# Optimization experiments

Hardware: AMD Instinct MI355X
Metric: run time of the kernel (lower is better)

Reference implementation:

```python
import jax, jax.numpy as jnp
import numpy as np

B, C, D, H, W = 4, 128, 16, 16, 16
C8 = C // 8
TEXT = 256
N = D * H * W


def setup_inputs() -> dict:
    key = jax.random.key(0)
    ks = jax.random.split(key, 13)
    s = lambda fan: 1.0 / np.sqrt(fan)
    return {
        "x": jax.random.normal(ks[0], (B, C, D, H, W), jnp.float32),
        "text_emb": jax.random.normal(ks[1], (B, TEXT), jnp.float32),
        "Wq": jax.random.normal(ks[2], (C8, C), jnp.float32) * s(C),
        "bq": jax.random.normal(ks[3], (C8,), jnp.float32) * 0.01,
        "Wk": jax.random.normal(ks[4], (C8, C), jnp.float32) * s(C),
        "bk": jax.random.normal(ks[5], (C8,), jnp.float32) * 0.01,
        "Wv": jax.random.normal(ks[6], (C, C), jnp.float32) * s(C),
        "bv": jax.random.normal(ks[7], (C,), jnp.float32) * 0.01,
        "Wtk": jax.random.normal(ks[8], (C8, TEXT), jnp.float32) * s(TEXT),
        "btk": jax.random.normal(ks[9], (C8,), jnp.float32) * 0.01,
        "Wtv": jax.random.normal(ks[10], (C, TEXT), jnp.float32) * s(TEXT),
        "btv": jax.random.normal(ks[11], (C,), jnp.float32) * 0.01,
        # gamma is zero-init in the original; use a nonzero value so the
        # attention path contributes to the output (and to gradients).
        "gamma": jax.random.normal(ks[12], (1,), jnp.float32) * 0.1 + 0.5,
    }


def reference(x, text_emb, Wq, bq, Wk, bk, Wv, bv, Wtk, btk, Wtv, btv, gamma):
    b, c, d, h, w = x.shape
    n = d * h * w
    xf = x.reshape(b, c, n)                       # [B, C, N]
    # 1x1x1 convs == channel matmuls
    q = jnp.einsum('oc,bcn->bno', Wq, xf) + bq    # [B, N, C8]
    k = jnp.einsum('oc,bcn->bon', Wk, xf) + bk[None, :, None]  # [B, C8, N]
    v = jnp.einsum('oc,bcn->bon', Wv, xf) + bv[None, :, None]  # [B, C, N]
    # text-conditioned additive key/value (broadcast over all voxels)
    tk = (text_emb @ Wtk.T + btk)[:, :, None]     # [B, C8, 1]
    tv = (text_emb @ Wtv.T + btv)[:, :, None]     # [B, C, 1]
    k = k + tk
    v = v + tv
    # unscaled attention: softmax over keys
    scores = jnp.einsum('bno,bom->bnm', q, k)     # [B, N, N]
    attn = jax.nn.softmax(scores, axis=-1)
    # out[b,c,n] = sum_m v[b,c,m] * attn[b,n,m]
    out = jnp.einsum('bcm,bnm->bcn', v, attn).reshape(b, c, d, h, w)
    return gamma * out + x
```

## Files before the change

### kernel.cpp

```cpp
#include <hip/hip_runtime.h>
#include <math.h>

#define BB 4
#define CC 128
#define C8 16
#define TEXTN 256
#define NN 4096
#define WQB 64
#define NT 32

typedef __attribute__((ext_vector_type(8))) __bf16 bf16x8;
typedef __attribute__((ext_vector_type(16))) float f32x16;

#define LOG2E 1.44269504088896340736f

static __device__ __forceinline__ ushort f2bf(float f) {
  unsigned u = __builtin_bit_cast(unsigned, f);
  u += 0x7FFFu + ((u >> 16) & 1u);
  return (ushort)(u >> 16);
}

static __device__ __forceinline__ float exp2a(float x) {
#if __has_builtin(__builtin_amdgcn_exp2f)
  return __builtin_amdgcn_exp2f(x);
#else
  return exp2f(x);
#endif
}

static __device__ __forceinline__ unsigned cvt_pk_bf16(float lo, float hi) {
  unsigned r;
  asm("v_cvt_pk_bf16_f32 %0, %1, %2" : "=v"(r) : "v"(lo), "v"(hi));
  return r;
}
static __device__ __forceinline__ void pl32swap(unsigned &a, unsigned &b) {
  asm("v_permlane32_swap_b32 %0, %1" : "+v"(a), "+v"(b));
}

__global__ __launch_bounds__(256) void k_text(
    const float* __restrict__ text, const float* __restrict__ Wtk,
    const float* __restrict__ btk, const float* __restrict__ Wtv,
    const float* __restrict__ btv, float* __restrict__ tkv) {
  __shared__ float ts[TEXTN];
  int b = blockIdx.x;
  for (int i = threadIdx.x; i < TEXTN; i += 256) ts[i] = text[b * TEXTN + i];
  __syncthreads();
  int o = threadIdx.x;
  if (o < 144) {
    const float* w;
    float acc;
    if (o < 16) { w = Wtk + o * TEXTN; acc = btk[o]; }
    else        { w = Wtv + (o - 16) * TEXTN; acc = btv[o - 16]; }
    #pragma unroll 8
    for (int t = 0; t < TEXTN; t++) acc += w[t] * ts[t];
    tkv[b * 144 + o] = acc;
  }
}

__global__ __launch_bounds__(320) void k_qkv(
    const float* __restrict__ x,
    const float* __restrict__ Wq, const float* __restrict__ bq,
    const float* __restrict__ Wk, const float* __restrict__ bk,
    const float* __restrict__ Wv, const float* __restrict__ bv,
    const float* __restrict__ tkv,
    ushort* __restrict__ qt, ushort* __restrict__ kt, ushort* __restrict__ vtB) {
  __shared__ __align__(16) ushort xs[64 * 128];
  int b = blockIdx.x >> 6;
  int n0 = (blockIdx.x & 63) * 64;
  int t = threadIdx.x;
  int w = t >> 6, lane = t & 63, l31 = lane & 31, hi = lane >> 5;

  for (int i = t; i < 1024; i += 320) {
    int n = i & 63, ch = i >> 6;
    union { ushort u[8]; uint4 v; } pk;
    #pragma unroll
    for (int j = 0; j < 8; ++j)
      pk.u[j] = f2bf(x[((size_t)b * CC + ch * 8 + j) * NN + n0 + n]);
    *(uint4*)&xs[n * 128 + ((ch ^ (n & 15)) << 3)] = pk.v;
  }

  const float* wrow;
  if (w == 0) wrow = (l31 < 16) ? (Wq + l31 * CC) : (Wk + (l31 - 16) * CC);
  else        wrow = Wv + (size_t)(32 * (w - 1) + l31) * CC;
  bf16x8 af[8];
  #pragma unroll
  for (int ks = 0; ks < 8; ++ks) {
    float4 u0 = *(const float4*)&wrow[ks * 16 + hi * 8];
    float4 u1 = *(const float4*)&wrow[ks * 16 + hi * 8 + 4];
    union { ushort u[8]; bf16x8 v; } tmp;
    tmp.u[0] = f2bf(u0.x); tmp.u[1] = f2bf(u0.y); tmp.u[2] = f2bf(u0.z); tmp.u[3] = f2bf(u0.w);
    tmp.u[4] = f2bf(u1.x); tmp.u[5] = f2bf(u1.y); tmp.u[6] = f2bf(u1.z); tmp.u[7] = f2bf(u1.w);
    af[ks] = tmp.v;
  }
  float badd[16];
  #pragma unroll
  for (int r = 0; r < 16; ++r) {
    int ol = (r & 3) + 8 * (r >> 2) + 4 * hi;
    if (w == 0) badd[r] = (ol < 16) ? bq[ol] : (bk[ol - 16] + tkv[b * 144 + ol - 16]);
    else { int c = 32 * (w - 1) + ol; badd[r] = bv[c] + tkv[b * 144 + 16 + c]; }
  }
  __syncthreads();

  #pragma unroll
  for (int n32 = 0; n32 < 2; ++n32) {
    int n = n32 * 32 + l31;
    int ng = n0 + n;
    bf16x8 bf[8];
    #pragma unroll
    for (int ks = 0; ks < 8; ++ks)
      bf[ks] = *(const bf16x8*)&xs[n * 128 + (((ks * 2 + hi) ^ (n & 15)) << 3)];
    f32x16 d;
    #pragma unroll
    for (int r = 0; r < 16; ++r) d[r] = 0.f;
    #pragma unroll
    for (int ks = 0; ks < 8; ++ks)
      d = __builtin_amdgcn_mfma_f32_32x32x16_bf16(af[ks], bf[ks], d, 0, 0, 0);
    #pragma unroll
    for (int g = 0; g < 4; ++g) {
      int o0 = 8 * g + 4 * hi;
      float v0 = d[g * 4 + 0] + badd[g * 4 + 0];
      float v1 = d[g * 4 + 1] + badd[g * 4 + 1];
      float v2 = d[g * 4 + 2] + badd[g * 4 + 2];
      float v3 = d[g * 4 + 3] + badd[g * 4 + 3];
      if (w == 0 && o0 < 16) { v0 *= LOG2E; v1 *= LOG2E; v2 *= LOG2E; v3 *= LOG2E; }
      ushort4 pkv;
      pkv.x = f2bf(v0); pkv.y = f2bf(v1); pkv.z = f2bf(v2); pkv.w = f2bf(v3);
      if (w == 0) {
        if (o0 < 16) *(ushort4*)&qt[(b * NN + ng) * C8 + o0] = pkv;
        else         *(ushort4*)&kt[(b * NN + ng) * C8 + o0 - 16] = pkv;
      } else {
        int c0 = 32 * (w - 1) + o0;
        int base = b * (NN / 8) * CC * 8 + (ng >> 3) * (CC * 8) + (ng & 7);
        vtB[base + (c0 + 0) * 8] = pkv.x;
        vtB[base + (c0 + 1) * 8] = pkv.y;
        vtB[base + (c0 + 2) * 8] = pkv.z;
        vtB[base + (c0 + 3) * 8] = pkv.w;
      }
    }
  }
}

__global__ __launch_bounds__(512) void k_attn(
    const ushort* __restrict__ qt, const ushort* __restrict__ kt,
    const ushort* __restrict__ vtB, const float* __restrict__ x,
    const float* __restrict__ gamma_p, float* __restrict__ out) {
  __shared__ __align__(16) float mergeAcc[4][2][1024];
  __shared__ float mergeL[4][2][2][32];
  __shared__ float invGL[64];

  int b = blockIdx.x >> 6;
  int q0 = (blockIdx.x & 63) * WQB;
  int t = threadIdx.x;
  int w = t >> 6, lane = t & 63, l31 = lane & 31, hi = lane >> 5;
  int ms = w >> 1, ch = w & 1;

  const ushort* ktb = kt + (size_t)b * NN * C8;
  const ushort* vbb = vtB + (size_t)b * (NN / 8) * CC * 8;

  bf16x8 qfA = *(const bf16x8*)&qt[((size_t)b * NN + q0 + l31) * C8 + hi * 8];
  bf16x8 qfB = *(const bf16x8*)&qt[((size_t)b * NN + q0 + 32 + l31) * C8 + hi * 8];

  f32x16 accA0, accA1, accB0, accB1;
  #pragma unroll
  for (int r = 0; r < 16; ++r) { accA0[r] = 0.f; accA1[r] = 0.f; accB0[r] = 0.f; accB1[r] = 0.f; }
  float lpA = 0.f, lpB = 0.f;

  f32x16 z;
  #pragma unroll
  for (int r = 0; r < 16; ++r) z[r] = 0.f;

  const ushort* kp  = ktb + (ms * 32 + l31) * C8 + hi * 8;
  const ushort* vp0 = vbb + (size_t)(ms * 4 + 0 + hi) * (CC * 8) + (ch * 64 + l31) * 8;
  const ushort* vp1 = vbb + (size_t)(ms * 4 + 2 + hi) * (CC * 8) + (ch * 64 + l31) * 8;

  bf16x8 kfA, kfB;
  kfA = *(const bf16x8*)kp; kp += 128 * C8;

#define MKPF(P, OUT0, OUT1)                                                   \
  {                                                                           \
    unsigned a0 = cvt_pk_bf16(P[0], P[1]), b0 = cvt_pk_bf16(P[4], P[5]);      \
    unsigned c0 = cvt_pk_bf16(P[2], P[3]), d0 = cvt_pk_bf16(P[6], P[7]);      \
    pl32swap(a0, b0); pl32swap(c0, d0);                                       \
    union { unsigned u[4]; bf16x8 v; } u0; u0.u[0] = a0; u0.u[1] = c0;        \
    u0.u[2] = b0; u0.u[3] = d0; OUT0 = u0.v;                                  \
    unsigned a1 = cvt_pk_bf16(P[8], P[9]), b1 = cvt_pk_bf16(P[12], P[13]);    \
    unsigned c1 = cvt_pk_bf16(P[10], P[11]), d1 = cvt_pk_bf16(P[14], P[15]);  \
    pl32swap(a1, b1); pl32swap(c1, d1);                                       \
    union { unsigned u[4]; bf16x8 v; } u1; u1.u[0] = a1; u1.u[1] = c1;        \
    u1.u[2] = b1; u1.u[3] = d1; OUT1 = u1.v;                                  \
  }

#define STEP(CK, NK)                                                          \
  {                                                                           \
    NK = *(const bf16x8*)kp; kp += 128 * C8;                                  \
    bf16x8 vA0 = *(const bf16x8*)(vp0);                   \
    bf16x8 vA1 = *(const bf16x8*)(vp0 + 256);             \
    bf16x8 vB0 = *(const bf16x8*)(vp1);                   \
    bf16x8 vB1 = *(const bf16x8*)(vp1 + 256);             \
    vp0 += 16 * CC * 8; vp1 += 16 * CC * 8;                                   \
    f32x16 sA = __builtin_amdgcn_mfma_f32_32x32x16_bf16(CK, qfA, z, 0, 0, 0); \
    f32x16 sB = __builtin_amdgcn_mfma_f32_32x32x16_bf16(CK, qfB, z, 0, 0, 0); \
    float pA[16], pB[16];                                                     \
    _Pragma("unroll")                                                         \
    for (int r = 0; r < 16; ++r) pA[r] = exp2a(sA[r]);                        \
    _Pragma("unroll")                                                         \
    for (int r = 0; r < 16; ++r) pB[r] = exp2a(sB[r]);                        \
    {                                                                         \
      float y0 = (pA[0] + pA[1]) + (pA[2] + pA[3]);                           \
      float y1 = (pA[4] + pA[5]) + (pA[6] + pA[7]);                           \
      float y2 = (pA[8] + pA[9]) + (pA[10] + pA[11]);                         \
      float y3 = (pA[12] + pA[13]) + (pA[14] + pA[15]);                       \
      lpA += (y0 + y1) + (y2 + y3);                                           \
      float u0 = (pB[0] + pB[1]) + (pB[2] + pB[3]);                           \
      float u1 = (pB[4] + pB[5]) + (pB[6] + pB[7]);                           \
      float u2 = (pB[8] + pB[9]) + (pB[10] + pB[11]);                         \
      float u3 = (pB[12] + pB[13]) + (pB[14] + pB[15]);                       \
      lpB += (u0 + u1) + (u2 + u3);                                           \
    }                                                                         \
    bf16x8 pfA0, pfA1, pfB0, pfB1;                                            \
    MKPF(pA, pfA0, pfA1)                                                      \
    MKPF(pB, pfB0, pfB1)                                                      \
    __builtin_amdgcn_s_setprio(1);                                            \
    accA0 = __builtin_amdgcn_mfma_f32_32x32x16_bf16(vA0, pfA0, accA0, 0, 0, 0); \
    accA1 = __builtin_amdgcn_mfma_f32_32x32x16_bf16(vA1, pfA0, accA1, 0, 0, 0); \
    accB0 = __builtin_amdgcn_mfma_f32_32x32x16_bf16(vA0, pfB0, accB0, 0, 0, 0); \
    accB1 = __builtin_amdgcn_mfma_f32_32x32x16_bf16(vA1, pfB0, accB1, 0, 0, 0); \
    accA0 = __builtin_amdgcn_mfma_f32_32x32x16_bf16(vB0, pfA1, accA0, 0, 0, 0); \
    accA1 = __builtin_amdgcn_mfma_f32_32x32x16_bf16(vB1, pfA1, accA1, 0, 0, 0); \
    accB0 = __builtin_amdgcn_mfma_f32_32x32x16_bf16(vB0, pfB1, accB0, 0, 0, 0); \
    accB1 = __builtin_amdgcn_mfma_f32_32x32x16_bf16(vB1, pfB1, accB1, 0, 0, 0); \
    __builtin_amdgcn_s_setprio(0);                                            \
  }

  for (int tt = 0; tt < NT; tt += 2) {
    STEP(kfA, kfB)
    STEP(kfB, kfA)
  }
#undef STEP
#undef MKPF

  if (ch == 0) {
    mergeL[ms][hi][0][l31] = lpA;
    mergeL[ms][hi][1][l31] = lpB;
  }
  __syncthreads();
  if (t < 64) {
    float L = 0.f;
    #pragma unroll
    for (int m2 = 0; m2 < 4; ++m2)
      #pragma unroll
      for (int h2 = 0; h2 < 2; ++h2) L += mergeL[m2][h2][t >> 5][t & 31];
    invGL[t] = gamma_p[0] / L;
  }

#define EPI(ACC, QT, CB, FIRST)                                               \
  {                                                                           \
    if (!(FIRST)) __syncthreads();                                            \
    _Pragma("unroll")                                                         \
    for (int r = 0; r < 16; ++r)                                              \
      mergeAcc[ms][ch][(((r & 3) + 8 * (r >> 2) + 4 * hi) << 5) | l31] = ACC[r]; \
    __syncthreads();                                                          \
    int idx = t * 4;                                                          \
    int qq = idx & 31, cl = idx >> 5;                                         \
    int chh = cl >> 5, crow = cl & 31;                                        \
    float4 sum = *(const float4*)&mergeAcc[0][chh][crow * 32 + qq];           \
    _Pragma("unroll")                                                         \
    for (int m2 = 1; m2 < 4; ++m2) {                                          \
      float4 sv = *(const float4*)&mergeAcc[m2][chh][crow * 32 + qq];         \
      sum.x += sv.x; sum.y += sv.y; sum.z += sv.z; sum.w += sv.w;             \
    }                                                                         \
    float4 gl = *(const float4*)&invGL[(QT) * 32 + qq];                       \
    int c = chh * 64 + (CB) * 32 + crow;                                      \
    size_t base = ((size_t)b * CC + c) * NN + q0 + (QT) * 32 + qq;            \
    float4 xv = *(const float4*)&x[base];                                     \
    float4 ov;                                                                \
    ov.x = sum.x * gl.x + xv.x;                                               \
    ov.y = sum.y * gl.y + xv.y;                                               \
    ov.z = sum.z * gl.z + xv.z;                                               \
    ov.w = sum.w * gl.w + xv.w;                                               \
    *(float4*)&out[base] = ov;                                                \
  }

  EPI(accA0, 0, 0, 1)
  EPI(accA1, 0, 1, 0)
  EPI(accB0, 1, 0, 0)
  EPI(accB1, 1, 1, 0)
#undef EPI
}

extern "C" void kernel_launch(void* const* d_in, const int* in_sizes, int n_in,
                              void* d_out, int out_size, void* d_ws, size_t ws_size,
                              hipStream_t stream) {
  const float* x     = (const float*)d_in[0];
  const float* text  = (const float*)d_in[1];
  const float* Wq    = (const float*)d_in[2];
  const float* bq    = (const float*)d_in[3];
  const float* Wk    = (const float*)d_in[4];
  const float* bk    = (const float*)d_in[5];
  const float* Wv    = (const float*)d_in[6];
  const float* bv    = (const float*)d_in[7];
  const float* Wtk   = (const float*)d_in[8];
  const float* btk   = (const float*)d_in[9];
  const float* Wtv   = (const float*)d_in[10];
  const float* btv   = (const float*)d_in[11];
  const float* gamma = (const float*)d_in[12];
  float* outp = (float*)d_out;

  char* wsb = (char*)d_ws;
  float*  tkv = (float*)wsb;
  ushort* qt  = (ushort*)(wsb + 4096);
  ushort* kt  = (ushort*)(wsb + 4096 + 524288);
  ushort* vtB = (ushort*)(wsb + 4096 + 2 * 524288);

  k_text<<<BB, 256, 0, stream>>>(text, Wtk, btk, Wtv, btv, tkv);
  k_qkv<<<BB * NN / 64, 320, 0, stream>>>(x, Wq, bq, Wk, bk, Wv, bv, tkv, qt, kt, vtB);
  k_attn<<<BB * NN / WQB, 512, 0, stream>>>(qt, kt, vtB, x, gamma, outp);
}
```

Measured before the change: 52.89 us.

## Split attention over channel halves with LDS-staged V and shared P tiles

Doubles the attention grid by splitting output channels into two halves per block. Each warp now computes scores for one 32-query tile instead of two and shares its bf16 probabilities through LDS. V tiles are double-buffered into LDS with global_load_lds instead of being read directly from global memory. Block indices are swizzled across XCDs. The aim is more parallelism and less per-warp exp/score work, at the cost of a barrier every key step and recomputing QK scores and exps once for each channel half.

```diff
diff --git a/kernel.cpp b/kernel.cpp
--- a/kernel.cpp
+++ b/kernel.cpp
@@ -35,6 +35,12 @@
 }
 static __device__ __forceinline__ void pl32swap(unsigned &a, unsigned &b) {
   asm("v_permlane32_swap_b32 %0, %1" : "+v"(a), "+v"(b));
+}
+
+static __device__ __forceinline__ void gl_lds16(const ushort* g, ushort* l) {
+  __builtin_amdgcn_global_load_lds(
+      (const __attribute__((address_space(1))) unsigned*)g,
+      (__attribute__((address_space(3))) unsigned*)l, 16, 0, 0);
 }
 
 __global__ __launch_bounds__(256) void k_text(
@@ -144,133 +150,135 @@
     const ushort* __restrict__ qt, const ushort* __restrict__ kt,
     const ushort* __restrict__ vtB, const float* __restrict__ x,
     const float* __restrict__ gamma_p, float* __restrict__ out) {
-  __shared__ __align__(16) float mergeAcc[4][2][1024];
-  __shared__ float mergeL[4][2][2][32];
-  __shared__ float invGL[64];
-
-  int b = blockIdx.x >> 6;
-  int q0 = (blockIdx.x & 63) * WQB;
+  __shared__ __align__(16) char smem[49152];
+  ushort* Vb = (ushort*)smem;
+  ushort* Pb = (ushort*)(smem + 32768);
+  float* mergeAcc = (float*)smem;
+  float* mergeLf  = (float*)(smem + 32768);
+  float* invGLf   = (float*)(smem + 32768 + 2048);
+
+  int raw = blockIdx.x;
+  int swz = (raw & 7) * 64 + (raw >> 3);
+  int b = swz >> 7, chalf = (swz >> 6) & 1, q0 = (swz & 63) * WQB;
   int t = threadIdx.x;
   int w = t >> 6, lane = t & 63, l31 = lane & 31, hi = lane >> 5;
   int ms = w >> 1, ch = w & 1;
 
-  const ushort* ktb = kt + (size_t)b * NN * C8;
-  const ushort* vbb = vtB + (size_t)b * (NN / 8) * CC * 8;
-
-  bf16x8 qfA = *(const bf16x8*)&qt[((size_t)b * NN + q0 + l31) * C8 + hi * 8];
-  bf16x8 qfB = *(const bf16x8*)&qt[((size_t)b * NN + q0 + 32 + l31) * C8 + hi * 8];
-
-  f32x16 accA0, accA1, accB0, accB1;
-  #pragma unroll
-  for (int r = 0; r < 16; ++r) { accA0[r] = 0.f; accA1[r] = 0.f; accB0[r] = 0.f; accB1[r] = 0.f; }
-  float lpA = 0.f, lpB = 0.f;
+  const ushort* ktb  = kt + (size_t)b * NN * C8;
+  const ushort* vsrc = vtB + (size_t)b * (NN / 8) * CC * 8 + chalf * 64 * 8;
+
+  bf16x8 qf = *(const bf16x8*)&qt[((size_t)b * NN + q0 + ch * 32 + l31) * C8 + hi * 8];
+
+  f32x16 acc0, acc1;
+  #pragma unroll
+  for (int r = 0; r < 16; ++r) { acc0[r] = 0.f; acc1[r] = 0.f; }
+  float lp = 0.f;
 
   f32x16 z;
   #pragma unroll
   for (int r = 0; r < 16; ++r) z[r] = 0.f;
 
-  const ushort* kp  = ktb + (ms * 32 + l31) * C8 + hi * 8;
-  const ushort* vp0 = vbb + (size_t)(ms * 4 + 0 + hi) * (CC * 8) + (ch * 64 + l31) * 8;
-  const ushort* vp1 = vbb + (size_t)(ms * 4 + 2 + hi) * (CC * 8) + (ch * 64 + l31) * 8;
-
-  bf16x8 kfA, kfB;
-  kfA = *(const bf16x8*)kp; kp += 128 * C8;
-
-#define MKPF(P, OUT0, OUT1)                                                   \
+#define STAGE(STEP, BUF)                                                      \
   {                                                                           \
-    unsigned a0 = cvt_pk_bf16(P[0], P[1]), b0 = cvt_pk_bf16(P[4], P[5]);      \
-    unsigned c0 = cvt_pk_bf16(P[2], P[3]), d0 = cvt_pk_bf16(P[6], P[7]);      \
-    pl32swap(a0, b0); pl32swap(c0, d0);                                       \
-    union { unsigned u[4]; bf16x8 v; } u0; u0.u[0] = a0; u0.u[1] = c0;        \
-    u0.u[2] = b0; u0.u[3] = d0; OUT0 = u0.v;                                  \
-    unsigned a1 = cvt_pk_bf16(P[8], P[9]), b1 = cvt_pk_bf16(P[12], P[13]);    \
-    unsigned c1 = cvt_pk_bf16(P[10], P[11]), d1 = cvt_pk_bf16(P[14], P[15]);  \
-    pl32swap(a1, b1); pl32swap(c1, d1);                                       \
-    union { unsigned u[4]; bf16x8 v; } u1; u1.u[0] = a1; u1.u[1] = c1;        \
-    u1.u[2] = b1; u1.u[3] = d1; OUT1 = u1.v;                                  \
-  }
-
-#define STEP(CK, NK)                                                          \
-  {                                                                           \
-    NK = *(const bf16x8*)kp; kp += 128 * C8;                                  \
-    bf16x8 vA0 = *(const bf16x8*)(vp0);                   \
-    bf16x8 vA1 = *(const bf16x8*)(vp0 + 256);             \
-    bf16x8 vB0 = *(const bf16x8*)(vp1);                   \
-    bf16x8 vB1 = *(const bf16x8*)(vp1 + 256);             \
-    vp0 += 16 * CC * 8; vp1 += 16 * CC * 8;                                   \
-    f32x16 sA = __builtin_amdgcn_mfma_f32_32x32x16_bf16(CK, qfA, z, 0, 0, 0); \
-    f32x16 sB = __builtin_amdgcn_mfma_f32_32x32x16_bf16(CK, qfB, z, 0, 0, 0); \
-    float pA[16], pB[16];                                                     \
-    _Pragma("unroll")                                                         \
-    for (int r = 0; r < 16; ++r) pA[r] = exp2a(sA[r]);                        \
-    _Pragma("unroll")                                                         \
-    for (int r = 0; r < 16; ++r) pB[r] = exp2a(sB[r]);                        \
-    {                                                                         \
-      float y0 = (pA[0] + pA[1]) + (pA[2] + pA[3]);                           \
-      float y1 = (pA[4] + pA[5]) + (pA[6] + pA[7]);                           \
-      float y2 = (pA[8] + pA[9]) + (pA[10] + pA[11]);                         \
-      float y3 = (pA[12] + pA[13]) + (pA[14] + pA[15]);                       \
-      lpA += (y0 + y1) + (y2 + y3);                                           \
-      float u0 = (pB[0] + pB[1]) + (pB[2] + pB[3]);                           \
-      float u1 = (pB[4] + pB[5]) + (pB[6] + pB[7]);                           \
-      float u2 = (pB[8] + pB[9]) + (pB[10] + pB[11]);                         \
-      float u3 = (pB[12] + pB[13]) + (pB[14] + pB[15]);                       \
-      lpB += (u0 + u1) + (u2 + u3);                                           \
-    }                                                                         \
-    bf16x8 pfA0, pfA1, pfB0, pfB1;                                            \
-    MKPF(pA, pfA0, pfA1)                                                      \
-    MKPF(pB, pfB0, pfB1)                                                      \
-    __builtin_amdgcn_s_setprio(1);                                            \
-    accA0 = __builtin_amdgcn_mfma_f32_32x32x16_bf16(vA0, pfA0, accA0, 0, 0, 0); \
-    accA1 = __builtin_amdgcn_mfma_f32_32x32x16_bf16(vA1, pfA0, accA1, 0, 0, 0); \
-    accB0 = __builtin_amdgcn_mfma_f32_32x32x16_bf16(vA0, pfB0, accB0, 0, 0, 0); \
-    accB1 = __builtin_amdgcn_mfma_f32_32x32x16_bf16(vA1, pfB0, accB1, 0, 0, 0); \
-    accA0 = __builtin_amdgcn_mfma_f32_32x32x16_bf16(vB0, pfA1, accA0, 0, 0, 0); \
-    accA1 = __builtin_amdgcn_mfma_f32_32x32x16_bf16(vB1, pfA1, accA1, 0, 0, 0); \
-    accB0 = __builtin_amdgcn_mfma_f32_32x32x16_bf16(vB0, pfB1, accB0, 0, 0, 0); \
-    accB1 = __builtin_amdgcn_mfma_f32_32x32x16_bf16(vB1, pfB1, accB1, 0, 0, 0); \
-    __builtin_amdgcn_s_setprio(0);                                            \
-  }
-
-  for (int tt = 0; tt < NT; tt += 2) {
-    STEP(kfA, kfB)
-    STEP(kfB, kfA)
-  }
-#undef STEP
-#undef MKPF
-
-  if (ch == 0) {
-    mergeL[ms][hi][0][l31] = lpA;
-    mergeL[ms][hi][1][l31] = lpB;
-  }
+    int cg = (STEP) << 4;                                                     \
+    gl_lds16(vsrc + ((size_t)(cg + (t >> 6)) * CC + (t & 63)) * 8,            \
+             Vb + (BUF) * 8192 + t * 8);                                      \
+    gl_lds16(vsrc + ((size_t)(cg + 8 + (t >> 6)) * CC + (t & 63)) * 8,        \
+             Vb + (BUF) * 8192 + (t + 512) * 8);                              \
+  }
+
+#define LDK(T) (*(const bf16x8*)&ktb[((T) * 128 + ms * 32 + l31) * C8 + hi * 8])
+#define LDVF(CUR, KS) (*(const bf16x8*)&Vb[(CUR) * 8192 + ((ms * 4 + (KS) * 2 + hi) * 64 + (ch * 32 + l31)) * 8])
+#define PSLOT(MS, QT, KS) ((bf16x8*)&Pb[((((MS) * 2 + (QT)) * 2 + (KS)) * 64 + lane) * 8])
+
+  STAGE(0, 0)
+  bf16x8 kf = LDK(0);
+  __syncthreads();
+
+  for (int tt = 0; tt < NT; ++tt) {
+    int cur = tt & 1;
+    int tn = (tt + 1) & (NT - 1);
+    STAGE(tn, cur ^ 1)
+    bf16x8 kfn = LDK(tn);
+    bf16x8 vf0 = LDVF(cur, 0);
+    bf16x8 vf1 = LDVF(cur, 1);
+
+    f32x16 s = __builtin_amdgcn_mfma_f32_32x32x16_bf16(kf, qf, z, 0, 0, 0);
+    float p[16];
+    #pragma unroll
+    for (int r = 0; r < 16; ++r) p[r] = exp2a(s[r]);
+    {
+      float y0 = (p[0] + p[1]) + (p[2] + p[3]);
+      float y1 = (p[4] + p[5]) + (p[6] + p[7]);
+      float y2 = (p[8] + p[9]) + (p[10] + p[11]);
+      float y3 = (p[12] + p[13]) + (p[14] + p[15]);
+      lp += (y0 + y1) + (y2 + y3);
+    }
+    {
+      unsigned a0 = cvt_pk_bf16(p[0], p[1]), b0 = cvt_pk_bf16(p[4], p[5]);
+      unsigned c0 = cvt_pk_bf16(p[2], p[3]), d0 = cvt_pk_bf16(p[6], p[7]);
+      pl32swap(a0, b0); pl32swap(c0, d0);
+      union { unsigned u[4]; bf16x8 v; } u0; u0.u[0] = a0; u0.u[1] = c0;
+      u0.u[2] = b0; u0.u[3] = d0;
+      *PSLOT(ms, ch, 0) = u0.v;
+      unsigned a1 = cvt_pk_bf16(p[8], p[9]), b1 = cvt_pk_bf16(p[12], p[13]);
+      unsigned c1 = cvt_pk_bf16(p[10], p[11]), d1 = cvt_pk_bf16(p[14], p[15]);
+      pl32swap(a1, b1); pl32swap(c1, d1);
+      union { unsigned u[4]; bf16x8 v; } u1; u1.u[0] = a1; u1.u[1] = c1;
+      u1.u[2] = b1; u1.u[3] = d1;
+      *PSLOT(ms, ch, 1) = u1.v;
+    }
+    asm volatile("s_waitcnt lgkmcnt(0)" ::: "memory");
+    __builtin_amdgcn_s_barrier();
+
+    bf16x8 pA0 = *PSLOT(ms, 0, 0);
+    bf16x8 pA1 = *PSLOT(ms, 0, 1);
+    bf16x8 pB0 = *PSLOT(ms, 1, 0);
+    bf16x8 pB1 = *PSLOT(ms, 1, 1);
+
+    __builtin_amdgcn_s_setprio(1);
+    acc0 = __builtin_amdgcn_mfma_f32_32x32x16_bf16(vf0, pA0, acc0, 0, 0, 0);
+    acc0 = __builtin_amdgcn_mfma_f32_32x32x16_bf16(vf1, pA1, acc0, 0, 0, 0);
+    acc1 = __builtin_amdgcn_mfma_f32_32x32x16_bf16(vf0, pB0, acc1, 0, 0, 0);
+    acc1 = __builtin_amdgcn_mfma_f32_32x32x16_bf16(vf1, pB1, acc1, 0, 0, 0);
+    __builtin_amdgcn_s_setprio(0);
+
+    kf = kfn;
+    __syncthreads();
+  }
+#undef STAGE
+#undef LDK
+#undef LDVF
+#undef PSLOT
+
+  mergeLf[(((ms * 2 + ch) * 2 + hi) << 5) + l31] = lp;
   __syncthreads();
   if (t < 64) {
     float L = 0.f;
     #pragma unroll
     for (int m2 = 0; m2 < 4; ++m2)
       #pragma unroll
-      for (int h2 = 0; h2 < 2; ++h2) L += mergeL[m2][h2][t >> 5][t & 31];
-    invGL[t] = gamma_p[0] / L;
-  }
-
-#define EPI(ACC, QT, CB, FIRST)                                               \
+      for (int h2 = 0; h2 < 2; ++h2)
+        L += mergeLf[(((m2 * 2 + (t >> 5)) * 2 + h2) << 5) + (t & 31)];
+    invGLf[t] = gamma_p[0] / L;
+  }
+
+#define EPI(ACC, QT)                                                          \
   {                                                                           \
-    if (!(FIRST)) __syncthreads();                                            \
     _Pragma("unroll")                                                         \
     for (int r = 0; r < 16; ++r)                                              \
-      mergeAcc[ms][ch][(((r & 3) + 8 * (r >> 2) + 4 * hi) << 5) | l31] = ACC[r]; \
+      mergeAcc[((ms * 64) + ch * 32 + ((r & 3) + 8 * (r >> 2) + 4 * hi)) * 32 + l31] = ACC[r]; \
     __syncthreads();                                                          \
     int idx = t * 4;                                                          \
     int qq = idx & 31, cl = idx >> 5;                                         \
-    int chh = cl >> 5, crow = cl & 31;                                        \
-    float4 sum = *(const float4*)&mergeAcc[0][chh][crow * 32 + qq];           \
+    float4 sum = *(const float4*)&mergeAcc[(0 * 64 + cl) * 32 + qq];          \
     _Pragma("unroll")                                                         \
     for (int m2 = 1; m2 < 4; ++m2) {                                          \
-      float4 sv = *(const float4*)&mergeAcc[m2][chh][crow * 32 + qq];         \
+      float4 sv = *(const float4*)&mergeAcc[(m2 * 64 + cl) * 32 + qq];        \
       sum.x += sv.x; sum.y += sv.y; sum.z += sv.z; sum.w += sv.w;             \
     }                                                                         \
-    float4 gl = *(const float4*)&invGL[(QT) * 32 + qq];                       \
-    int c = chh * 64 + (CB) * 32 + crow;                                      \
+    float4 gl = *(const float4*)&invGLf[(QT) * 32 + qq];                      \
+    int c = chalf * 64 + cl;                                                  \
     size_t base = ((size_t)b * CC + c) * NN + q0 + (QT) * 32 + qq;            \
     float4 xv = *(const float4*)&x[base];                                     \
     float4 ov;                                                                \
@@ -279,12 +287,11 @@
     ov.z = sum.z * gl.z + xv.z;                                               \
     ov.w = sum.w * gl.w + xv.w;                                               \
     *(float4*)&out[base] = ov;                                                \
-  }
-
-  EPI(accA0, 0, 0, 1)
-  EPI(accA1, 0, 1, 0)
-  EPI(accB0, 1, 0, 0)
-  EPI(accB1, 1, 1, 0)
+    __syncthreads();                                                          \
+  }
+
+  EPI(acc0, 0)
+  EPI(acc1, 1)
 #undef EPI
 }
 
@@ -314,5 +321,5 @@
 
   k_text<<<BB, 256, 0, stream>>>(text, Wtk, btk, Wtv, btv, tkv);
   k_qkv<<<BB * NN / 64, 320, 0, stream>>>(x, Wq, bq, Wk, bk, Wv, bv, tkv, qt, kt, vtB);
-  k_attn<<<BB * NN / WQB, 512, 0, stream>>>(qt, kt, vtB, x, gamma, outp);
-}
+  k_attn<<<BB * (NN / WQB) * 2, 512, 0, stream>>>(qt, kt, vtB, x, gamma, outp);
+}
```

Measured after the change: 57.97 us. 1.1x slower.
